# Kernel tuning notes

Measured on AMD Instinct MI355X. Metric: run time of the kernel, lower is better.

## Reference

```python
import jax, jax.numpy as jnp
import numpy as np

N_NODES = 100000
N_EDGES = 1600000
F_IN = 64
HID = 64
N_CLASSES = 47


def lgconv(x, src, dst, n_nodes):
    # PyG LGConv: symmetric gcn_norm WITHOUT self-loops, sum aggregation.
    ones = jnp.ones(src.shape[0], dtype=x.dtype)
    deg = jax.ops.segment_sum(ones, dst, num_segments=n_nodes)  # in-degree at targets
    dinv = jnp.where(deg > 0, jax.lax.rsqrt(jnp.maximum(deg, 1.0)), 0.0)
    norm = dinv[src] * dinv[dst]  # [E]
    msg = x[src] * norm[:, None]  # [E, F] gathered messages
    return jax.ops.segment_sum(msg, dst, num_segments=n_nodes)  # [N, F]


def setup_inputs() -> dict:
    key = jax.random.key(0)
    k1, k2, k3, k4 = jax.random.split(key, 4)
    x = jax.random.normal(k1, (N_NODES, F_IN), dtype=jnp.float32)
    edge_index = jax.random.randint(k2, (2, N_EDGES), 0, N_NODES, dtype=jnp.int64)
    W1 = jax.random.normal(k3, (F_IN, HID), dtype=jnp.float32) * (1.0 / np.sqrt(F_IN))
    b1 = jnp.zeros((HID,), dtype=jnp.float32)
    W2 = jax.random.normal(k4, (HID, N_CLASSES), dtype=jnp.float32) * (1.0 / np.sqrt(HID))
    b2 = jnp.zeros((N_CLASSES,), dtype=jnp.float32)
    return {"x": x, "edge_index": edge_index, "W1": W1, "b1": b1, "W2": W2, "b2": b2}


def reference(x, edge_index, W1, b1, W2, b2):
    src, dst = edge_index[0], edge_index[1]
    h = jax.nn.relu(lgconv(x, src, dst, N_NODES))          # conv1 + relu (dropout = id in eval)
    h = jax.nn.relu(h @ W1 + b1)                           # lin1 + relu
    h = jax.nn.relu(lgconv(h, src, dst, N_NODES))          # conv2 + relu
    logits = h @ W2 + b2                                   # lin2
    return jax.nn.log_softmax(logits, axis=-1)
```

## Files before the change

### kernel.cpp

```cpp
#include <hip/hip_runtime.h>
#include <hip/hip_fp16.h>
#include <math.h>

#define NN 100000
#define F 64
#define NC 47
#define NSUP 391
#define SUPR 256
#define ACHUNK 4096
#define PAD 5120

__global__ __launch_bounds__(256) void binA_direct_kernel(const void* __restrict__ ei,
                                                          int* __restrict__ superCnt,
                                                          unsigned* __restrict__ superArr,
                                                          int E) {
    __shared__ int2 ed[ACHUNK];
    __shared__ int h[512], gbase[512];
    __shared__ int is64_s;
    int t = threadIdx.x;
    if (t < 64) {
        int v = ((const int*)ei)[2 * t + 1];
        unsigned long long ball = __ballot(v == 0);
        if (t == 0) is64_s = (ball == ~0ULL) ? 1 : 0;
    }
    h[t] = 0; h[t + 256] = 0;
    __syncthreads();
    bool is64 = (is64_s != 0);
    int cb = blockIdx.x * ACHUNK;
    int ce = min(cb + ACHUNK, E);
    for (int i = cb + t; i < ce; i += 256) {
        int s, d;
        if (is64) {
            s = (int)((const long long*)ei)[i];
            d = (int)((const long long*)ei)[(size_t)E + i];
        } else {
            s = ((const int*)ei)[i];
            d = ((const int*)ei)[(size_t)E + i];
        }
        ed[i - cb] = make_int2(s, d);
        atomicAdd(&h[d >> 8], 1);
    }
    __syncthreads();
    for (int b = t; b < 512; b += 256) {
        int c = h[b];
        gbase[b] = (b < NSUP && c > 0) ? atomicAdd(&superCnt[b], c) : 0;
        h[b] = 0;
    }
    __syncthreads();
    int nloc = ce - cb;
    for (int i = t; i < nloc; i += 256) {
        int2 e = ed[i];
        int sup = e.y >> 8;
        int pos = atomicAdd(&h[sup], 1);
        unsigned pk = (unsigned)e.x | ((unsigned)(e.y & (SUPR - 1)) << 17);
        superArr[(size_t)sup * PAD + gbase[sup] + pos] = pk;
    }
}

__global__ __launch_bounds__(512) void superscan_kernel(const int* __restrict__ superCnt,
                                                        int* __restrict__ superBase) {
    __shared__ int sc[512];
    int t = threadIdx.x;
    int v = (t < NSUP) ? superCnt[t] : 0;
    sc[t] = v;
    __syncthreads();
    for (int off = 1; off < 512; off <<= 1) {
        int a = (t >= off) ? sc[t - off] : 0;
        __syncthreads();
        sc[t] += a;
        __syncthreads();
    }
    if (t < NSUP) superBase[t] = sc[t] - v;
    if (t == NSUP - 1) superBase[NSUP] = sc[t];
}

__global__ __launch_bounds__(256) void binB_kernel(const unsigned* __restrict__ superArr,
                                                   const int* __restrict__ superCnt,
                                                   const int* __restrict__ superBase,
                                                   int* __restrict__ rowptr,
                                                   float* __restrict__ dinv,
                                                   unsigned* __restrict__ esrc, int E) {
    __shared__ int hist[256];
    __shared__ int cur[256];
    __shared__ int wsum[4], wbase[4];
    int s = blockIdx.x, t = threadIdx.x;
    int wb = superBase[s];
    int cnt = superCnt[s];
    const unsigned* arr = superArr + (size_t)s * PAD;
    hist[t] = 0;
    __syncthreads();
    for (int i = t; i < cnt; i += 256)
        atomicAdd(&hist[(arr[i] >> 17) & (SUPR - 1)], 1);
    __syncthreads();
    int myv = hist[t];
    int lane = t & 63, w = t >> 6;
    int v = myv;
#pragma unroll
    for (int off = 1; off < 64; off <<= 1) {
        int u = __shfl_up(v, off, 64);
        if (lane >= off) v += u;
    }
    if (lane == 63) wsum[w] = v;
    __syncthreads();
    if (t == 0) {
        int r = 0;
#pragma unroll
        for (int j = 0; j < 4; ++j) { wbase[j] = r; r += wsum[j]; }
    }
    __syncthreads();
    int excl = v + wbase[w] - myv;
    int gr = s * SUPR + t;
    if (gr < NN) {
        rowptr[gr] = wb + excl;
        dinv[gr] = (myv > 0) ? rsqrtf((float)myv) : 0.0f;
    }
    if (s == NSUP - 1 && t == 0) rowptr[NN] = E;
    cur[t] = excl;
    __syncthreads();
    for (int i = t; i < cnt; i += 256) {
        unsigned e = arr[i];
        int r = (e >> 17) & (SUPR - 1);
        int pos = atomicAdd(&cur[r], 1);
        esrc[wb + pos] = e & 0x1FFFFu;
    }
}

__global__ void f2h_scale_kernel(const float4* __restrict__ in4,
                                 const float* __restrict__ dinv,
                                 uint2* __restrict__ outh, int n4) {
    int i = blockIdx.x * blockDim.x + threadIdx.x;
    if (i >= n4) return;
    float dv = dinv[i >> 4];
    float4 v = in4[i];
    __half2 h01 = __floats2half2_rn(v.x * dv, v.y * dv);
    __half2 h23 = __floats2half2_rn(v.z * dv, v.w * dv);
    uint2 r;
    r.x = *(const unsigned*)&h01;
    r.y = *(const unsigned*)&h23;
    outh[i] = r;
}

__global__ __launch_bounds__(256) void conv_ps_kernel(const uint2* __restrict__ xh,
                                                      const int* __restrict__ rowptr,
                                                      const unsigned* __restrict__ esrc,
                                                      const float* __restrict__ dinv,
                                                      uint2* __restrict__ outh, int n) {
    int row = blockIdx.x * 4 + (threadIdx.x >> 6);
    if (row >= n) return;
    int lane = threadIdx.x & 63;
    int es = lane >> 4, f4 = lane & 15;
    int beg = rowptr[row], end = rowptr[row + 1];
    float4 acc = make_float4(0.f, 0.f, 0.f, 0.f);
    for (int base = beg; base < end; base += 64) {
        int m = end - base;
        if (m > 64) m = 64;
        int pk = (lane < m) ? (int)esrc[base + lane] : 0;
        int iters = (m + 3) >> 2;
        int k = 0;
        for (; k + 4 <= iters; k += 4) {
            int i0 = 4 * k + es, i1 = i0 + 4, i2 = i0 + 8, i3 = i0 + 12;
            int s0 = __shfl(pk, i0, 64);
            int s1 = __shfl(pk, i1, 64);
            int s2 = __shfl(pk, i2, 64);
            int s3 = __shfl(pk, i3, 64);
            float w0 = (i0 < m) ? 1.0f : 0.0f;
            float w1 = (i1 < m) ? 1.0f : 0.0f;
            float w2 = (i2 < m) ? 1.0f : 0.0f;
            float w3 = (i3 < m) ? 1.0f : 0.0f;
            uint2 v0 = xh[(size_t)s0 * 16 + f4];
            uint2 v1 = xh[(size_t)s1 * 16 + f4];
            uint2 v2 = xh[(size_t)s2 * 16 + f4];
            uint2 v3 = xh[(size_t)s3 * 16 + f4];
            float2 a01 = __half22float2(*reinterpret_cast<const __half2*>(&v0.x));
            float2 a23 = __half22float2(*reinterpret_cast<const __half2*>(&v0.y));
            acc.x = fmaf(a01.x, w0, acc.x); acc.y = fmaf(a01.y, w0, acc.y);
            acc.z = fmaf(a23.x, w0, acc.z); acc.w = fmaf(a23.y, w0, acc.w);
            float2 b01 = __half22float2(*reinterpret_cast<const __half2*>(&v1.x));
            float2 b23 = __half22float2(*reinterpret_cast<const __half2*>(&v1.y));
            acc.x = fmaf(b01.x, w1, acc.x); acc.y = fmaf(b01.y, w1, acc.y);
            acc.z = fmaf(b23.x, w1, acc.z); acc.w = fmaf(b23.y, w1, acc.w);
            float2 c01 = __half22float2(*reinterpret_cast<const __half2*>(&v2.x));
            float2 c23 = __half22float2(*reinterpret_cast<const __half2*>(&v2.y));
            acc.x = fmaf(c01.x, w2, acc.x); acc.y = fmaf(c01.y, w2, acc.y);
            acc.z = fmaf(c23.x, w2, acc.z); acc.w = fmaf(c23.y, w2, acc.w);
            float2 d01 = __half22float2(*reinterpret_cast<const __half2*>(&v3.x));
            float2 d23 = __half22float2(*reinterpret_cast<const __half2*>(&v3.y));
            acc.x = fmaf(d01.x, w3, acc.x); acc.y = fmaf(d01.y, w3, acc.y);
            acc.z = fmaf(d23.x, w3, acc.z); acc.w = fmaf(d23.y, w3, acc.w);
        }
        for (; k < iters; ++k) {
            int i0 = 4 * k + es;
            int s0 = __shfl(pk, i0, 64);
            float w0 = (i0 < m) ? 1.0f : 0.0f;
            uint2 v0 = xh[(size_t)s0 * 16 + f4];
            float2 a01 = __half22float2(*reinterpret_cast<const __half2*>(&v0.x));
            float2 a23 = __half22float2(*reinterpret_cast<const __half2*>(&v0.y));
            acc.x = fmaf(a01.x, w0, acc.x); acc.y = fmaf(a01.y, w0, acc.y);
            acc.z = fmaf(a23.x, w0, acc.z); acc.w = fmaf(a23.y, w0, acc.w);
        }
    }
#pragma unroll
    for (int off = 16; off <= 32; off <<= 1) {
        acc.x += __shfl_xor(acc.x, off, 64);
        acc.y += __shfl_xor(acc.y, off, 64);
        acc.z += __shfl_xor(acc.z, off, 64);
        acc.w += __shfl_xor(acc.w, off, 64);
    }
    if (es == 0) {
        float dv = dinv[row];
        __half2 h01 = __floats2half2_rn(acc.x * dv, acc.y * dv);
        __half2 h23 = __floats2half2_rn(acc.z * dv, acc.w * dv);
        uint2 r;
        r.x = *(const unsigned*)&h01;
        r.y = *(const unsigned*)&h23;
        outh[(size_t)row * 16 + f4] = r;
    }
}

__device__ __forceinline__ float4 h4_to_f4_relu(uint2 hv) {
    float2 a01 = __half22float2(*reinterpret_cast<const __half2*>(&hv.x));
    float2 a23 = __half22float2(*reinterpret_cast<const __half2*>(&hv.y));
    return make_float4(fmaxf(a01.x, 0.f), fmaxf(a01.y, 0.f),
                       fmaxf(a23.x, 0.f), fmaxf(a23.y, 0.f));
}

__global__ __launch_bounds__(256) void lin1_kernel(const uint2* __restrict__ h2,
                                                   const float* __restrict__ W1,
                                                   const float* __restrict__ b1,
                                                   const float* __restrict__ dinv,
                                                   __half* __restrict__ outh, int n) {
    __shared__ float wt[64 * 64];
    __shared__ float ht[64 * 64];
    int t = threadIdx.x;
    for (int i = t; i < 64 * 64; i += 256) {
        int k = i >> 6, c = i & 63;
        int kq = k >> 2, slot = kq ^ (c & 7);
        wt[c * 64 + slot * 4 + (k & 3)] = W1[i];
    }
    int row0 = blockIdx.x * 64;
    float4* ht4 = (float4*)ht;
#pragma unroll
    for (int j = 0; j < 4; ++j) {
        int flat = t + 256 * j;
        int r = flat >> 4;
        int kq = flat & 15;
        int gr = row0 + r;
        float4 v = (gr < n) ? h4_to_f4_relu(h2[(size_t)gr * 16 + kq])
                            : make_float4(0.f, 0.f, 0.f, 0.f);
        ht4[r * 16 + (kq ^ ((r >> 2) & 7))] = v;
    }
    __syncthreads();
    const float4* wt4 = (const float4*)wt;
    const float4* ht4c = (const float4*)ht;

    int tx = t & 15, ty = t >> 4;
    float acc[4][4] = {};
#pragma unroll 2
    for (int kq = 0; kq < 16; ++kq) {
        int wslot = kq ^ (tx & 7);
        float4 b0 = wt4[(tx +  0) * 16 + wslot];
        float4 b1v = wt4[(tx + 16) * 16 + wslot];
        float4 b2v = wt4[(tx + 32) * 16 + wslot];
        float4 b3v = wt4[(tx + 48) * 16 + wslot];
        int aslot = kq ^ (ty & 7);
#pragma unroll
        for (int i = 0; i < 4; ++i) {
            float4 a = ht4c[(4 * ty + i) * 16 + aslot];
            acc[i][0] = fmaf(a.x, b0.x,  fmaf(a.y, b0.y,  fmaf(a.z, b0.z,  fmaf(a.w, b0.w,  acc[i][0]))));
            acc[i][1] = fmaf(a.x, b1v.x, fmaf(a.y, b1v.y, fmaf(a.z, b1v.z, fmaf(a.w, b1v.w, acc[i][1]))));
            acc[i][2] = fmaf(a.x, b2v.x, fmaf(a.y, b2v.y, fmaf(a.z, b2v.z, fmaf(a.w, b2v.w, acc[i][2]))));
            acc[i][3] = fmaf(a.x, b3v.x, fmaf(a.y, b3v.y, fmaf(a.z, b3v.z, fmaf(a.w, b3v.w, acc[i][3]))));
        }
    }
    float bj[4];
#pragma unroll
    for (int g = 0; g < 4; ++g) bj[g] = b1[tx + 16 * g];
    int r0 = row0 + 4 * ty;
#pragma unroll
    for (int i = 0; i < 4; ++i) {
        int r = r0 + i;
        if (r >= n) break;
        float dv = dinv[r];
#pragma unroll
        for (int g = 0; g < 4; ++g)
            outh[(size_t)r * 64 + tx + 16 * g] =
                __float2half(fmaxf(acc[i][g] + bj[g], 0.0f) * dv);
    }
}

__global__ __launch_bounds__(256) void lin2_kernel(const uint2* __restrict__ h2,
                                                   const float* __restrict__ W2,
                                                   const float* __restrict__ b2,
                                                   float* __restrict__ out, int n) {
    __shared__ float wt[64 * 64];
    __shared__ float ht[64 * 64];
    int t = threadIdx.x;
    for (int i = t; i < 64 * 64; i += 256) {
        int k = i >> 6, c = i & 63;
        int kq = k >> 2, slot = kq ^ (c & 7);
        wt[c * 64 + slot * 4 + (k & 3)] = (c < NC) ? W2[k * NC + c] : 0.0f;
    }
    int row0 = blockIdx.x * 64;
    float4* ht4 = (float4*)ht;
#pragma unroll
    for (int j = 0; j < 4; ++j) {
        int flat = t + 256 * j;
        int r = flat >> 4;
        int kq = flat & 15;
        int gr = row0 + r;
        float4 v = (gr < n) ? h4_to_f4_relu(h2[(size_t)gr * 16 + kq])
                            : make_float4(0.f, 0.f, 0.f, 0.f);
        ht4[r * 16 + (kq ^ ((r >> 2) & 7))] = v;
    }
    __syncthreads();
    const float4* wt4 = (const float4*)wt;
    const float4* ht4c = (const float4*)ht;

    int tx = t & 15, ty = t >> 4;
    float acc[4][4] = {};
#pragma unroll 2
    for (int kq = 0; kq < 16; ++kq) {
        int wslot = kq ^ (tx & 7);
        float4 b0 = wt4[(tx +  0) * 16 + wslot];
        float4 b1v = wt4[(tx + 16) * 16 + wslot];
        float4 b2v = wt4[(tx + 32) * 16 + wslot];
        float4 b3v = wt4[(tx + 48) * 16 + wslot];
        int aslot = kq ^ (ty & 7);
#pragma unroll
        for (int i = 0; i < 4; ++i) {
            float4 a = ht4c[(4 * ty + i) * 16 + aslot];
            acc[i][0] = fmaf(a.x, b0.x,  fmaf(a.y, b0.y,  fmaf(a.z, b0.z,  fmaf(a.w, b0.w,  acc[i][0]))));
            acc[i][1] = fmaf(a.x, b1v.x, fmaf(a.y, b1v.y, fmaf(a.z, b1v.z, fmaf(a.w, b1v.w, acc[i][1]))));
            acc[i][2] = fmaf(a.x, b2v.x, fmaf(a.y, b2v.y, fmaf(a.z, b2v.z, fmaf(a.w, b2v.w, acc[i][2]))));
            acc[i][3] = fmaf(a.x, b3v.x, fmaf(a.y, b3v.y, fmaf(a.z, b3v.z, fmaf(a.w, b3v.w, acc[i][3]))));
        }
    }
    bool vm[4];
    float bj[4];
#pragma unroll
    for (int g = 0; g < 4; ++g) {
        int c = tx + 16 * g;
        vm[g] = (c < NC);
        bj[g] = vm[g] ? b2[c] : 0.0f;
    }
    int r0 = row0 + 4 * ty;
#pragma unroll
    for (int i = 0; i < 4; ++i) {
        int r = r0 + i;
        float v[4];
        float m = -INFINITY;
#pragma unroll
        for (int g = 0; g < 4; ++g) {
            v[g] = acc[i][g] + bj[g];
            if (vm[g]) m = fmaxf(m, v[g]);
        }
#pragma unroll
        for (int off = 8; off > 0; off >>= 1) m = fmaxf(m, __shfl_xor(m, off, 64));
        float s = 0.0f;
#pragma unroll
        for (int g = 0; g < 4; ++g)
            if (vm[g]) s += expf(v[g] - m);
#pragma unroll
        for (int off = 8; off > 0; off >>= 1) s += __shfl_xor(s, off, 64);
        float lse = m + logf(s);
        if (r < n) {
#pragma unroll
            for (int g = 0; g < 4; ++g)
                if (vm[g]) out[(size_t)r * NC + tx + 16 * g] = v[g] - lse;
        }
    }
}

extern "C" void kernel_launch(void* const* d_in, const int* in_sizes, int n_in,
                              void* d_out, int out_size, void* d_ws, size_t ws_size,
                              hipStream_t stream) {
    const float* x  = (const float*)d_in[0];
    const void*  ei = d_in[1];
    const float* W1 = (const float*)d_in[2];
    const float* b1 = (const float*)d_in[3];
    const float* W2 = (const float*)d_in[4];
    const float* b2 = (const float*)d_in[5];
    float* out = (float*)d_out;

    const int E = in_sizes[1] / 2;

    char* ws = (char*)d_ws;
    size_t off = 0;
    auto alloc = [&](size_t bytes) -> void* {
        void* p = ws + off;
        off = (off + bytes + 255) & ~(size_t)255;
        return p;
    };
    float*    dinv      = (float*)   alloc((size_t)NN * 4);
    int*      superCnt  = (int*)     alloc(512 * 4);
    int*      superBase = (int*)     alloc(512 * 4);
    unsigned* superArr  = (unsigned*)alloc((size_t)NSUP * PAD * 4);
    int*      rowptr    = (int*)     alloc((size_t)(NN + 1) * 4);
    unsigned* esrc      = (unsigned*)alloc((size_t)E * 4);
    uint2*    xh        = (uint2*)   alloc((size_t)NN * 16 * 8);
    __half*   bufAh     = (__half*)  alloc((size_t)NN * F * 2);
    __half*   bufBh     = (__half*)  alloc((size_t)NN * F * 2);

    hipMemsetAsync(superCnt, 0, 512 * 4, stream);

    binA_direct_kernel<<<(E + ACHUNK - 1) / ACHUNK, 256, 0, stream>>>(
        ei, superCnt, superArr, E);
    superscan_kernel<<<1, 512, 0, stream>>>(superCnt, superBase);
    binB_kernel<<<NSUP, 256, 0, stream>>>(
        superArr, superCnt, superBase, rowptr, dinv, esrc, E);

    f2h_scale_kernel<<<(NN * 16 + 255) / 256, 256, 0, stream>>>(
        (const float4*)x, dinv, xh, NN * 16);

    const int conv_blocks = (NN + 3) / 4;
    const int lin_blocks = (NN + 63) / 64;

    conv_ps_kernel<<<conv_blocks, 256, 0, stream>>>(xh, rowptr, esrc, dinv,
                                                    (uint2*)bufAh, NN);

    lin1_kernel<<<lin_blocks, 256, 0, stream>>>((const uint2*)bufAh, W1, b1, dinv,
                                                bufBh, NN);

    conv_ps_kernel<<<conv_blocks, 256, 0, stream>>>((const uint2*)bufBh, rowptr, esrc,
                                                    dinv, (uint2*)bufAh, NN);

    lin2_kernel<<<lin_blocks, 256, 0, stream>>>((const uint2*)bufAh, W2, b2, out, NN);
}
```

Measured before the change: 180.0 us.

## Fuse conv aggregation into linear kernels and fold fp16 scaling into binning

The x-to-fp16 scaled conversion is folded into the end of binB, so the separate f2h kernel goes away. Each conv aggregation now runs inside the following linear kernel: every wave aggregates 16 rows straight into shared memory before the matmul. This removes the intermediate fp16 buffer round trip and two launches. The cost is less parallelism during the gather, since there are 1563 blocks of 64 rows instead of 25000 blocks of 4 rows, and the gather loop runs serially per wave, which may hurt latency hiding.

```diff
diff --git a/kernel.cpp b/kernel.cpp
--- a/kernel.cpp
+++ b/kernel.cpp
@@ -77,11 +77,14 @@
 __global__ __launch_bounds__(256) void binB_kernel(const unsigned* __restrict__ superArr,
                                                    const int* __restrict__ superCnt,
                                                    const int* __restrict__ superBase,
+                                                   const float4* __restrict__ x4,
                                                    int* __restrict__ rowptr,
                                                    float* __restrict__ dinv,
-                                                   unsigned* __restrict__ esrc, int E) {
+                                                   unsigned* __restrict__ esrc,
+                                                   uint2* __restrict__ xh, int E) {
     __shared__ int hist[256];
     __shared__ int cur[256];
+    __shared__ float dloc[256];
     __shared__ int wsum[4], wbase[4];
     int s = blockIdx.x, t = threadIdx.x;
     int wb = superBase[s];
@@ -110,12 +113,14 @@
     __syncthreads();
     int excl = v + wbase[w] - myv;
     int gr = s * SUPR + t;
+    float dv = (myv > 0) ? rsqrtf((float)myv) : 0.0f;
     if (gr < NN) {
         rowptr[gr] = wb + excl;
-        dinv[gr] = (myv > 0) ? rsqrtf((float)myv) : 0.0f;
+        dinv[gr] = dv;
     }
     if (s == NSUP - 1 && t == 0) rowptr[NN] = E;
     cur[t] = excl;
+    dloc[t] = dv;
     __syncthreads();
     for (int i = t; i < cnt; i += 256) {
         unsigned e = arr[i];
@@ -123,32 +128,25 @@
         int pos = atomicAdd(&cur[r], 1);
         esrc[wb + pos] = e & 0x1FFFFu;
     }
-}
-
-__global__ void f2h_scale_kernel(const float4* __restrict__ in4,
-                                 const float* __restrict__ dinv,
-                                 uint2* __restrict__ outh, int n4) {
-    int i = blockIdx.x * blockDim.x + threadIdx.x;
-    if (i >= n4) return;
-    float dv = dinv[i >> 4];
-    float4 v = in4[i];
-    __half2 h01 = __floats2half2_rn(v.x * dv, v.y * dv);
-    __half2 h23 = __floats2half2_rn(v.z * dv, v.w * dv);
-    uint2 r;
-    r.x = *(const unsigned*)&h01;
-    r.y = *(const unsigned*)&h23;
-    outh[i] = r;
-}
-
-__global__ __launch_bounds__(256) void conv_ps_kernel(const uint2* __restrict__ xh,
-                                                      const int* __restrict__ rowptr,
-                                                      const unsigned* __restrict__ esrc,
-                                                      const float* __restrict__ dinv,
-                                                      uint2* __restrict__ outh, int n) {
-    int row = blockIdx.x * 4 + (threadIdx.x >> 6);
-    if (row >= n) return;
-    int lane = threadIdx.x & 63;
-    int es = lane >> 4, f4 = lane & 15;
+    int row0 = s * SUPR;
+    int nrow = min(SUPR, NN - row0);
+    for (int i = t; i < nrow * 16; i += 256) {
+        int rl = i >> 4;
+        float d = dloc[rl];
+        float4 vv = x4[(size_t)(row0 + rl) * 16 + (i & 15)];
+        __half2 h01 = __floats2half2_rn(vv.x * d, vv.y * d);
+        __half2 h23 = __floats2half2_rn(vv.z * d, vv.w * d);
+        uint2 r;
+        r.x = *(const unsigned*)&h01;
+        r.y = *(const unsigned*)&h23;
+        xh[(size_t)(row0 + rl) * 16 + (i & 15)] = r;
+    }
+}
+
+__device__ __forceinline__ float4 conv_row(const uint2* __restrict__ xh,
+                                           const int* __restrict__ rowptr,
+                                           const unsigned* __restrict__ esrc,
+                                           int row, int lane, int es, int f4) {
     int beg = rowptr[row], end = rowptr[row + 1];
     float4 acc = make_float4(0.f, 0.f, 0.f, 0.f);
     for (int base = beg; base < end; base += 64) {
@@ -206,29 +204,16 @@
         acc.z += __shfl_xor(acc.z, off, 64);
         acc.w += __shfl_xor(acc.w, off, 64);
     }
-    if (es == 0) {
-        float dv = dinv[row];
-        __half2 h01 = __floats2half2_rn(acc.x * dv, acc.y * dv);
-        __half2 h23 = __floats2half2_rn(acc.z * dv, acc.w * dv);
-        uint2 r;
-        r.x = *(const unsigned*)&h01;
-        r.y = *(const unsigned*)&h23;
-        outh[(size_t)row * 16 + f4] = r;
-    }
-}
-
-__device__ __forceinline__ float4 h4_to_f4_relu(uint2 hv) {
-    float2 a01 = __half22float2(*reinterpret_cast<const __half2*>(&hv.x));
-    float2 a23 = __half22float2(*reinterpret_cast<const __half2*>(&hv.y));
-    return make_float4(fmaxf(a01.x, 0.f), fmaxf(a01.y, 0.f),
-                       fmaxf(a23.x, 0.f), fmaxf(a23.y, 0.f));
-}
-
-__global__ __launch_bounds__(256) void lin1_kernel(const uint2* __restrict__ h2,
-                                                   const float* __restrict__ W1,
-                                                   const float* __restrict__ b1,
-                                                   const float* __restrict__ dinv,
-                                                   __half* __restrict__ outh, int n) {
+    return acc;
+}
+
+__global__ __launch_bounds__(256) void convlin1_kernel(const uint2* __restrict__ xh,
+                                                       const int* __restrict__ rowptr,
+                                                       const unsigned* __restrict__ esrc,
+                                                       const float* __restrict__ dinv,
+                                                       const float* __restrict__ W1,
+                                                       const float* __restrict__ b1,
+                                                       __half* __restrict__ outh, int n) {
     __shared__ float wt[64 * 64];
     __shared__ float ht[64 * 64];
     int t = threadIdx.x;
@@ -238,16 +223,20 @@
         wt[c * 64 + slot * 4 + (k & 3)] = W1[i];
     }
     int row0 = blockIdx.x * 64;
+    int w = t >> 6, lane = t & 63, es = lane >> 4, f4 = lane & 15;
     float4* ht4 = (float4*)ht;
-#pragma unroll
-    for (int j = 0; j < 4; ++j) {
-        int flat = t + 256 * j;
-        int r = flat >> 4;
-        int kq = flat & 15;
-        int gr = row0 + r;
-        float4 v = (gr < n) ? h4_to_f4_relu(h2[(size_t)gr * 16 + kq])
-                            : make_float4(0.f, 0.f, 0.f, 0.f);
-        ht4[r * 16 + (kq ^ ((r >> 2) & 7))] = v;
+    for (int rr = 0; rr < 16; ++rr) {
+        int rl = w * 16 + rr;
+        int row = row0 + rl;
+        float4 acc = make_float4(0.f, 0.f, 0.f, 0.f);
+        if (row < n) acc = conv_row(xh, rowptr, esrc, row, lane, es, f4);
+        if (es == 0) {
+            float dv = (row < n) ? dinv[row] : 0.0f;
+            float4 o;
+            o.x = fmaxf(acc.x * dv, 0.f); o.y = fmaxf(acc.y * dv, 0.f);
+            o.z = fmaxf(acc.z * dv, 0.f); o.w = fmaxf(acc.w * dv, 0.f);
+            ht4[rl * 16 + (f4 ^ ((rl >> 2) & 7))] = o;
+        }
     }
     __syncthreads();
     const float4* wt4 = (const float4*)wt;
@@ -288,10 +277,13 @@
     }
 }
 
-__global__ __launch_bounds__(256) void lin2_kernel(const uint2* __restrict__ h2,
-                                                   const float* __restrict__ W2,
-                                                   const float* __restrict__ b2,
-                                                   float* __restrict__ out, int n) {
+__global__ __launch_bounds__(256) void convlin2_kernel(const uint2* __restrict__ hh,
+                                                       const int* __restrict__ rowptr,
+                                                       const unsigned* __restrict__ esrc,
+                                                       const float* __restrict__ dinv,
+                                                       const float* __restrict__ W2,
+                                                       const float* __restrict__ b2,
+                                                       float* __restrict__ out, int n) {
     __shared__ float wt[64 * 64];
     __shared__ float ht[64 * 64];
     int t = threadIdx.x;
@@ -301,16 +293,20 @@
         wt[c * 64 + slot * 4 + (k & 3)] = (c < NC) ? W2[k * NC + c] : 0.0f;
     }
     int row0 = blockIdx.x * 64;
+    int w = t >> 6, lane = t & 63, es = lane >> 4, f4 = lane & 15;
     float4* ht4 = (float4*)ht;
-#pragma unroll
-    for (int j = 0; j < 4; ++j) {
-        int flat = t + 256 * j;
-        int r = flat >> 4;
-        int kq = flat & 15;
-        int gr = row0 + r;
-        float4 v = (gr < n) ? h4_to_f4_relu(h2[(size_t)gr * 16 + kq])
-                            : make_float4(0.f, 0.f, 0.f, 0.f);
-        ht4[r * 16 + (kq ^ ((r >> 2) & 7))] = v;
+    for (int rr = 0; rr < 16; ++rr) {
+        int rl = w * 16 + rr;
+        int row = row0 + rl;
+        float4 acc = make_float4(0.f, 0.f, 0.f, 0.f);
+        if (row < n) acc = conv_row(hh, rowptr, esrc, row, lane, es, f4);
+        if (es == 0) {
+            float dv = (row < n) ? dinv[row] : 0.0f;
+            float4 o;
+            o.x = fmaxf(acc.x * dv, 0.f); o.y = fmaxf(acc.y * dv, 0.f);
+            o.z = fmaxf(acc.z * dv, 0.f); o.w = fmaxf(acc.w * dv, 0.f);
+            ht4[rl * 16 + (f4 ^ ((rl >> 2) & 7))] = o;
+        }
     }
     __syncthreads();
     const float4* wt4 = (const float4*)wt;
@@ -398,7 +394,6 @@
     int*      rowptr    = (int*)     alloc((size_t)(NN + 1) * 4);
     unsigned* esrc      = (unsigned*)alloc((size_t)E * 4);
     uint2*    xh        = (uint2*)   alloc((size_t)NN * 16 * 8);
-    __half*   bufAh     = (__half*)  alloc((size_t)NN * F * 2);
     __half*   bufBh     = (__half*)  alloc((size_t)NN * F * 2);
 
     hipMemsetAsync(superCnt, 0, 512 * 4, stream);
@@ -407,22 +402,13 @@
         ei, superCnt, superArr, E);
     superscan_kernel<<<1, 512, 0, stream>>>(superCnt, superBase);
     binB_kernel<<<NSUP, 256, 0, stream>>>(
-        superArr, superCnt, superBase, rowptr, dinv, esrc, E);
-
-    f2h_scale_kernel<<<(NN * 16 + 255) / 256, 256, 0, stream>>>(
-        (const float4*)x, dinv, xh, NN * 16);
-
-    const int conv_blocks = (NN + 3) / 4;
+        superArr, superCnt, superBase, (const float4*)x, rowptr, dinv, esrc, xh, E);
+
     const int lin_blocks = (NN + 63) / 64;
 
-    conv_ps_kernel<<<conv_blocks, 256, 0, stream>>>(xh, rowptr, esrc, dinv,
-                                                    (uint2*)bufAh, NN);
-
-    lin1_kernel<<<lin_blocks, 256, 0, stream>>>((const uint2*)bufAh, W1, b1, dinv,
-                                                bufBh, NN);
-
-    conv_ps_kernel<<<conv_blocks, 256, 0, stream>>>((const uint2*)bufBh, rowptr, esrc,
-                                                    dinv, (uint2*)bufAh, NN);
-
-    lin2_kernel<<<lin_blocks, 256, 0, stream>>>((const uint2*)bufAh, W2, b2, out, NN);
-}
+    convlin1_kernel<<<lin_blocks, 256, 0, stream>>>(xh, rowptr, esrc, dinv,
+                                                    W1, b1, bufBh, NN);
+
+    convlin2_kernel<<<lin_blocks, 256, 0, stream>>>((const uint2*)bufBh, rowptr, esrc,
+                                                    dinv, W2, b2, out, NN);
+}
```

Result: slower. 223.8 us (+24.3%).
